# Kernel optimization log

Hardware: AMD Instinct MI355X
Metric: run time of the kernel (lower is better)

Reference implementation:

```python
import jax, jax.numpy as jnp
import numpy as np

# ---- layer_param constants (ihmehimmeli alpha-synapse defaults, see shape_source) ----
K_NO_SPIKE = 1000.0
DECAY_RATE = 1.0          # K in exp(K*t)
DECAY_RATE_INV = 1.0
FIRE_THRESHOLD = 1.0
IN_FEATURES = 1024
OUT_FEATURES = 512
N_PULSE = 10
BATCH = 32
MIN_W_ARG = -0.3678794411714423  # -1/e, domain boundary of Lambert W0


def lambertw0(x):
    """Principal branch Lambert W on [-1/e, 0], via Halley iterations."""
    e = jnp.exp(1.0)
    # series init near the branch point, w ~= x for small |x|
    w = jnp.where(x < -0.25,
                  -1.0 + jnp.sqrt(jnp.maximum(2.0 * (1.0 + e * x), 0.0)),
                  x * (1.0 - x))
    def halley(w, _):
        ew = jnp.exp(w)
        f = w * ew - x
        denom = ew * (w + 1.0) - (w + 2.0) * f / (2.0 * (w + 1.0) + 1e-12)
        w = w - f / (denom + 1e-12)
        return w, None
    w, _ = jax.lax.scan(halley, w, None, length=12)
    return w


def _alpha_solve(act, weight):
    """Causal-set cumulative spike-time solve for alpha synapses.
    act: [B,N] input spike times, weight: [O,N].
    V(t) = e^{-K t} (A t - B) with A = sum w e^{K t_i}, B = sum w t_i e^{K t_i};
    threshold crossing: t* = B/A - W0(-theta*K/A * e^{K B/A})/K,
    valid if t* lies between the last included and the next input spike.
    """
    order = jnp.argsort(act, axis=1)                             # [B,N]
    t_s = jnp.take_along_axis(act, order, axis=1)                # sorted spike times
    valid_in = t_s < K_NO_SPIKE
    z = jnp.where(valid_in, jnp.exp(DECAY_RATE * t_s), 0.0)      # exp of valid sorted spikes
    w_s = weight[:, order].transpose(1, 0, 2)                    # [B,O,N] weights in sorted order
    A_c = jnp.cumsum(w_s * z[:, None, :], axis=2)                # causal-set cumulative A
    B_c = jnp.cumsum(w_s * (z * t_s)[:, None, :], axis=2)        # causal-set cumulative B
    A_pos = A_c > 1e-10
    A_safe = jnp.where(A_pos, A_c, 1.0)
    b_over_a = B_c / A_safe
    arg = -FIRE_THRESHOLD * DECAY_RATE / A_safe * jnp.exp(jnp.minimum(DECAY_RATE * b_over_a, 80.0))
    lam_ok = A_pos & (arg >= MIN_W_ARG)
    wl = lambertw0(jnp.clip(arg, MIN_W_ARG, 0.0))
    t_cand = b_over_a - wl * DECAY_RATE_INV
    next_t = jnp.concatenate([t_s[:, 1:], jnp.full_like(t_s[:, :1], K_NO_SPIKE)], axis=1)
    valid = (lam_ok & valid_in[:, None, :]
             & (t_cand >= t_s[:, None, :]) & (t_cand <= next_t[:, None, :]))
    k_star = jnp.argmax(valid, axis=2)                           # first causal set that fires
    spiked = jnp.any(valid, axis=2)
    take = lambda m: jnp.take_along_axis(m, k_star[:, :, None], axis=2)[:, :, 0]
    spike_time = jnp.where(spiked, take(t_cand), K_NO_SPIKE)
    A = jnp.where(spiked, take(A_c), 1.0)
    Bv = jnp.where(spiked, take(B_c), 0.0)
    Wv = jnp.where(spiked, take(wl), 0.0)
    rank = jnp.argsort(order, axis=1)                            # position of each input in sorted order
    causal = rank[:, None, :] <= k_star[:, :, None]              # [B,O,N]
    return spike_time, A, Bv, Wv, causal


def setup_inputs() -> dict:
    key = jax.random.key(0)
    k1, k2 = jax.random.split(key)
    x = jax.random.uniform(k1, (BATCH, IN_FEATURES), dtype=jnp.float32)
    std = float(np.sqrt(2.0 / (IN_FEATURES + OUT_FEATURES)))
    weight = std * 7.0 + std * jax.random.normal(k2, (OUT_FEATURES, IN_FEATURES + N_PULSE), dtype=jnp.float32)
    pulse = jnp.linspace(0.0, 1.0, N_PULSE + 2, dtype=jnp.float32)[1:-1]
    return {"x": x, "weight": weight, "pulse": pulse}


def reference(x, weight, pulse):
    act = jnp.concatenate([x, jnp.broadcast_to(pulse[None, :], (x.shape[0], N_PULSE))], axis=1)
    spike_time, _, _, _, _ = _alpha_solve(act, weight)
    return spike_time
```

## Files before the change

kernel.cpp:

```cpp
#include <hip/hip_runtime.h>
#include <math.h>
#include <limits.h>

#define IN_FEATURES 1024
#define OUT_FEATURES 512
#define N_PULSE 10
#define NCOL 1034
#define BATCH 32
#define MIN_W_ARG -0.3678794411714423

#define NSEG 16
#define SEG 66
#define SCAN (NSEG * SEG)
#define TBLN 1088

#define OFF_TS  (TBLN * 4)
#define OFF_Z   (TBLN * 8)
#define OFF_ZT  (TBLN * 16)
#define TBL_BYTES (TBLN * 24)

#define PREP_T_BLOCKS 136
#define PREP_R_PARTS 5
#define PREP_BLOCKS (PREP_T_BLOCKS + BATCH * PREP_R_PARTS)

__global__ __launch_bounds__(256, 1) void prep_kernel(
        const float* __restrict__ w, float* __restrict__ wT,
        const float* __restrict__ x, const float* __restrict__ pulse,
        char* __restrict__ tbl) {
    __shared__ char smem_u[64 * 65 * 4];
    const int tid = threadIdx.x;

    if (blockIdx.x < PREP_T_BLOCKS) {
        float (*tile)[65] = (float (*)[65])smem_u;
        const int n0 = (blockIdx.x % 17) * 64;
        const int o0 = (blockIdx.x / 17) * 64;
        const int tx = tid & 63, ty = tid >> 6;
        #pragma unroll
        for (int r = 0; r < 16; ++r) {
            int ol = r * 4 + ty, n = n0 + tx;
            if (n < NCOL) tile[ol][tx] = w[(o0 + ol) * NCOL + n];
        }
        __syncthreads();
        #pragma unroll
        for (int r = 0; r < 16; ++r) {
            int nl = r * 4 + ty, n = n0 + nl;
            if (n < NCOL) wT[n * OUT_FEATURES + o0 + tx] = tile[tx][nl];
        }
    } else {
        unsigned long long* sk = (unsigned long long*)smem_u;
        float* keyf = (float*)(smem_u + TBLN * 8);
        const int rb = blockIdx.x - PREP_T_BLOCKS;
        const int b = rb / PREP_R_PARTS, part = rb % PREP_R_PARTS;

        for (int e = tid; e < TBLN; e += 256) {
            if (e < NCOL) {
                float t = (e < IN_FEATURES) ? x[b * IN_FEATURES + e]
                                            : pulse[e - IN_FEATURES];
                unsigned u = __float_as_uint(t);
                u = (u & 0x80000000u) ? ~u : (u | 0x80000000u);
                sk[e] = ((unsigned long long)u << 11) | (unsigned)e;
                keyf[e] = t;
            } else {
                sk[e] = 0xFFFFFFFFFFFFFFFFULL;
            }
        }
        __syncthreads();

        char* base = tbl + b * TBL_BYTES;
        int*    ordg = (int*)base;
        float*  tsg  = (float*)(base + OFF_TS);
        double* zg   = (double*)(base + OFF_Z);
        double* ztg  = (double*)(base + OFF_ZT);

        const int e = part * 256 + tid;
        if (e < NCOL) {
            unsigned long long mk = sk[e];
            int r = 0;
            for (int j0 = 0; j0 < TBLN; j0 += 16) {
                unsigned long long c[16];
                #pragma unroll
                for (int i = 0; i < 16; ++i) c[i] = sk[j0 + i];
                #pragma unroll
                for (int i = 0; i < 16; ++i) r += (c[i] < mk);
            }
            float t = keyf[e];
            double zv = exp((double)t);
            ordg[r] = e; tsg[r] = t; zg[r] = zv; ztg[r] = zv * (double)t;
        }
        if (part == PREP_R_PARTS - 1) {
            int p = 1024 + tid;
            if (p >= NCOL && p < TBLN) {
                ordg[p] = 0; tsg[p] = -1.0f; zg[p] = 0.0; ztg[p] = 0.0;
            }
        }
    }
}

__device__ __forceinline__ double lambertw0(double xx) {
    const double e = 2.718281828459045;
    double w = (xx < -0.25) ? (-1.0 + sqrt(fmax(2.0 * (1.0 + e * xx), 0.0)))
                            : xx * (1.0 - xx);
    #pragma unroll 4
    for (int i = 0; i < 12; ++i) {
        double ew = exp(w);
        double f  = w * ew - xx;
        double denom = ew * (w + 1.0) - (w + 2.0) * f / (2.0 * (w + 1.0) + 1e-12);
        w = w - f / (denom + 1e-12);
    }
    return w;
}

__global__ __launch_bounds__(1024) void solve_kernel(
        const float* __restrict__ wT,
        const char* __restrict__ tbl,
        float* __restrict__ out) {
    __shared__ char smem[TBL_BYTES];
    __shared__ double segA[NSEG * 64], segB[NSEG * 64];
    __shared__ int    sfk[NSEG * 64];
    __shared__ double sfA[NSEG * 64], sfB[NSEG * 64];

    const int b = blockIdx.x >> 3;
    const int o0 = (blockIdx.x & 7) << 6;
    const int wave = threadIdx.x >> 6;
    const int lane = threadIdx.x & 63;
    const int o = o0 + lane;

    {
        const uint4* g = (const uint4*)(tbl + b * TBL_BYTES);
        uint4* l = (uint4*)smem;
        for (int e = threadIdx.x; e < TBL_BYTES / 16; e += 1024) l[e] = g[e];
    }
    __syncthreads();
    const int*    ord_l = (const int*)smem;
    const float*  ts_l  = (const float*)(smem + OFF_TS);
    const double* z_l   = (const double*)(smem + OFF_Z);
    const double* zt_l  = (const double*)(smem + OFF_ZT);

    const int k0 = wave * SEG;

    {
        double a0 = 0.0, a1 = 0.0, b0 = 0.0, b1 = 0.0;
        for (int c = 0; c < SEG; c += 11) {
            int idx[11]; float buf[11];
            #pragma unroll
            for (int i = 0; i < 11; ++i) idx[i] = ord_l[k0 + c + i];
            #pragma unroll
            for (int i = 0; i < 11; ++i) buf[i] = wT[idx[i] * OUT_FEATURES + o];
            #pragma unroll
            for (int i = 0; i < 11; ++i) {
                double w = (double)buf[i];
                if (i & 1) { a1 = fma(w, z_l[k0 + c + i], a1);
                             b1 = fma(w, zt_l[k0 + c + i], b1); }
                else       { a0 = fma(w, z_l[k0 + c + i], a0);
                             b0 = fma(w, zt_l[k0 + c + i], b0); }
            }
        }
        segA[wave * 64 + lane] = a0 + a1;
        segB[wave * 64 + lane] = b0 + b1;
    }
    __syncthreads();

    {
        double A = 0.0, Bv = 0.0;
        for (int s = 0; s < wave; ++s) {
            A  += segA[s * 64 + lane];
            Bv += segB[s * 64 + lane];
        }
        int fk = INT_MAX; double fA = 0.0, fB = 0.0;
        for (int c = 0; c < SEG; c += 11) {
            int idx[11]; float buf[11];
            #pragma unroll
            for (int i = 0; i < 11; ++i) idx[i] = ord_l[k0 + c + i];
            #pragma unroll
            for (int i = 0; i < 11; ++i) buf[i] = wT[idx[i] * OUT_FEATURES + o];
            #pragma unroll
            for (int i = 0; i < 11; ++i) {
                int k = k0 + c + i;
                double w = (double)buf[i];
                A  = fma(w, z_l[k],  A);
                Bv = fma(w, zt_l[k], Bv);
                bool fire = (fk == INT_MAX) & (A > 1e-10) &
                            (fma(A, (double)ts_l[k + 1], -Bv) >= z_l[k + 1]);
                if (fire) { fk = k; fA = A; fB = Bv; }
            }
        }
        sfk[wave * 64 + lane] = fk;
        sfA[wave * 64 + lane] = fA;
        sfB[wave * 64 + lane] = fB;
    }
    __syncthreads();

    if (wave == 0) {
        int gk = INT_MAX; double gA = 0.0, gB = 0.0;
        #pragma unroll
        for (int s = 0; s < NSEG; ++s) {
            int k = sfk[s * 64 + lane];
            if (k < gk) { gk = k; gA = sfA[s * 64 + lane]; gB = sfB[s * 64 + lane]; }
        }
        bool done = (gk < NCOL);

        double AA, BB, tk, tn;
        bool have;
        if (done) {
            AA = gA; BB = gB;
            tk = (double)ts_l[gk];
            tn = (double)ts_l[gk + 1];
            have = true;
        } else {
            double tA = 0.0, tB = 0.0;
            #pragma unroll
            for (int s = 0; s < NSEG; ++s) { tA += segA[s * 64 + lane]; tB += segB[s * 64 + lane]; }
            AA = tA; BB = tB;
            tk = (double)ts_l[NCOL - 1];
            tn = 1000.0;
            have = (AA > 1e-10);
        }

        float result = 1000.0f;
        bool need_fb = false;
        if (have) {
            double boa = BB / AA;
            double arg = -exp(fmin(boa, 80.0)) / AA;
            if (arg >= MIN_W_ARG) {
                double wl = lambertw0(fmin(fmax(arg, MIN_W_ARG), 0.0));
                double tc = boa - wl;
                if (tc >= tk && tc <= tn) result = (float)tc;
                else need_fb = done;
            } else need_fb = done;
        }

        if (__ballot(need_fb) != 0ULL) {
            double A2 = gA, B2 = gB;
            for (int k = gk + 1; k < NCOL && k >= 0; ++k) {
                if (!need_fb) break;
                double w = (double)wT[ord_l[k] * OUT_FEATURES + o];
                A2 = fma(w, z_l[k], A2);
                B2 = fma(w, zt_l[k], B2);
                if (!(A2 > 1e-10)) continue;
                double tkk = (double)ts_l[k];
                double tnn = (k == NCOL - 1) ? 1000.0 : (double)ts_l[k + 1];
                double boa = B2 / A2;
                double arg = -exp(fmin(boa, 80.0)) / A2;
                if (arg >= MIN_W_ARG) {
                    double wl = lambertw0(fmin(fmax(arg, MIN_W_ARG), 0.0));
                    double tc = boa - wl;
                    if (tc >= tkk && tc <= tnn) { result = (float)tc; need_fb = false; }
                }
            }
        }
        out[b * OUT_FEATURES + o] = result;
    }
}

extern "C" void kernel_launch(void* const* d_in, const int* in_sizes, int n_in,
                              void* d_out, int out_size, void* d_ws, size_t ws_size,
                              hipStream_t stream) {
    const float* x      = (const float*)d_in[0];
    const float* weight = (const float*)d_in[1];
    const float* pulse  = (const float*)d_in[2];
    float* out = (float*)d_out;

    char* ws = (char*)d_ws;
    float* wT = (float*)ws;
    char*  tbl = ws + (size_t)NCOL * OUT_FEATURES * 4;

    hipLaunchKernelGGL(prep_kernel, dim3(PREP_BLOCKS), dim3(256), 0, stream,
                       weight, wT, x, pulse, tbl);
    hipLaunchKernelGGL(solve_kernel, dim3(BATCH * OUT_FEATURES / 64), dim3(1024), 0, stream,
                       wT, tbl, out);
}
```

Baseline: 91.48 us.

## Replace full rank-count sort with bucketed counting sort in prep kernel

Swaps the O(N^2) all-pairs rank count (spread over 5 blocks per batch row) for a bucket sort in one block per batch: histogram into 1024 buckets by value, prefix-scan, scatter, then rank each element only against others in its own bucket. This cuts the per-element comparison work in the prep stage. The bucket mapping assumes inputs lie in [0,1), which holds for uniform x and pulse values, and heavily skewed distributions would degrade it back toward quadratic within a bucket. Ties are still broken by index, so the ordering stays the same.

```diff
diff --git a/kernel.cpp b/kernel.cpp
--- a/kernel.cpp
+++ b/kernel.cpp
@@ -11,7 +11,6 @@
 
 #define NSEG 16
 #define SEG 66
-#define SCAN (NSEG * SEG)
 #define TBLN 1088
 
 #define OFF_TS  (TBLN * 4)
@@ -20,14 +19,21 @@
 #define TBL_BYTES (TBLN * 24)
 
 #define PREP_T_BLOCKS 136
-#define PREP_R_PARTS 5
-#define PREP_BLOCKS (PREP_T_BLOCKS + BATCH * PREP_R_PARTS)
+#define PREP_BLOCKS (PREP_T_BLOCKS + BATCH)
+
+#define R_KM   0
+#define R_KF   4136
+#define R_SIDX 8272
+#define R_BASE 12408
+#define R_RUN  16508
+#define R_PS   20604
+#define R_BYTES 21632
 
 __global__ __launch_bounds__(256, 1) void prep_kernel(
         const float* __restrict__ w, float* __restrict__ wT,
         const float* __restrict__ x, const float* __restrict__ pulse,
         char* __restrict__ tbl) {
-    __shared__ char smem_u[64 * 65 * 4];
+    __shared__ __align__(16) char smem_u[R_BYTES];
     const int tid = threadIdx.x;
 
     if (blockIdx.x < PREP_T_BLOCKS) {
@@ -47,51 +53,79 @@
             if (n < NCOL) wT[n * OUT_FEATURES + o0 + tx] = tile[tx][nl];
         }
     } else {
-        unsigned long long* sk = (unsigned long long*)smem_u;
-        float* keyf = (float*)(smem_u + TBLN * 8);
-        const int rb = blockIdx.x - PREP_T_BLOCKS;
-        const int b = rb / PREP_R_PARTS, part = rb % PREP_R_PARTS;
-
-        for (int e = tid; e < TBLN; e += 256) {
-            if (e < NCOL) {
-                float t = (e < IN_FEATURES) ? x[b * IN_FEATURES + e]
-                                            : pulse[e - IN_FEATURES];
-                unsigned u = __float_as_uint(t);
-                u = (u & 0x80000000u) ? ~u : (u | 0x80000000u);
-                sk[e] = ((unsigned long long)u << 11) | (unsigned)e;
-                keyf[e] = t;
-            } else {
-                sk[e] = 0xFFFFFFFFFFFFFFFFULL;
+        unsigned*  km   = (unsigned*)(smem_u + R_KM);
+        float*     kf   = (float*)(smem_u + R_KF);
+        int*       sidx = (int*)(smem_u + R_SIDX);
+        int*       base = (int*)(smem_u + R_BASE);
+        int*       run  = (int*)(smem_u + R_RUN);
+        int*       ps   = (int*)(smem_u + R_PS);
+        const int b = blockIdx.x - PREP_T_BLOCKS;
+
+        for (int e = tid; e < NCOL; e += 256) {
+            float t = (e < IN_FEATURES) ? x[b * IN_FEATURES + e]
+                                        : pulse[e - IN_FEATURES];
+            kf[e] = t;
+            unsigned u = __float_as_uint(t);
+            km[e] = (u & 0x80000000u) ? ~u : (u | 0x80000000u);
+        }
+        for (int i = tid; i < 1024; i += 256) run[i] = 0;
+        __syncthreads();
+
+        for (int e = tid; e < NCOL; e += 256) {
+            int bk = min(1023, max(0, (int)(kf[e] * 1024.0f)));
+            atomicAdd(&run[bk], 1);
+        }
+        __syncthreads();
+
+        int c4[4], v = 0;
+        #pragma unroll
+        for (int j = 0; j < 4; ++j) { c4[j] = run[4 * tid + j]; v += c4[j]; }
+        ps[tid] = v;
+        __syncthreads();
+        for (int off = 1; off < 256; off <<= 1) {
+            int xv = (tid >= off) ? ps[tid - off] : 0;
+            __syncthreads();
+            ps[tid] += xv;
+            __syncthreads();
+        }
+        int ex = ps[tid] - v;
+        #pragma unroll
+        for (int j = 0; j < 4; ++j) { base[4 * tid + j] = ex; ex += c4[j]; }
+        if (tid == 255) base[1024] = ex;
+        __syncthreads();
+        for (int i = tid; i < 1024; i += 256) run[i] = base[i];
+        __syncthreads();
+
+        for (int e = tid; e < NCOL; e += 256) {
+            int bk = min(1023, max(0, (int)(kf[e] * 1024.0f)));
+            int slot = atomicAdd(&run[bk], 1);
+            sidx[slot] = e;
+        }
+        __syncthreads();
+
+        char* gb = tbl + b * TBL_BYTES;
+        int*    ordg = (int*)gb;
+        float*  tsg  = (float*)(gb + OFF_TS);
+        double* zg   = (double*)(gb + OFF_Z);
+        double* ztg  = (double*)(gb + OFF_ZT);
+
+        for (int s = tid; s < NCOL; s += 256) {
+            int e = sidx[s];
+            float t = kf[e];
+            unsigned u = km[e];
+            int bk = min(1023, max(0, (int)(t * 1024.0f)));
+            int lo = base[bk], hi = base[bk + 1];
+            int r = lo;
+            for (int j = lo; j < hi; ++j) {
+                int ej = sidx[j];
+                unsigned uj = km[ej];
+                r += (uj < u) || (uj == u && ej < e);
             }
-        }
-        __syncthreads();
-
-        char* base = tbl + b * TBL_BYTES;
-        int*    ordg = (int*)base;
-        float*  tsg  = (float*)(base + OFF_TS);
-        double* zg   = (double*)(base + OFF_Z);
-        double* ztg  = (double*)(base + OFF_ZT);
-
-        const int e = part * 256 + tid;
-        if (e < NCOL) {
-            unsigned long long mk = sk[e];
-            int r = 0;
-            for (int j0 = 0; j0 < TBLN; j0 += 16) {
-                unsigned long long c[16];
-                #pragma unroll
-                for (int i = 0; i < 16; ++i) c[i] = sk[j0 + i];
-                #pragma unroll
-                for (int i = 0; i < 16; ++i) r += (c[i] < mk);
-            }
-            float t = keyf[e];
             double zv = exp((double)t);
             ordg[r] = e; tsg[r] = t; zg[r] = zv; ztg[r] = zv * (double)t;
         }
-        if (part == PREP_R_PARTS - 1) {
-            int p = 1024 + tid;
-            if (p >= NCOL && p < TBLN) {
-                ordg[p] = 0; tsg[p] = -1.0f; zg[p] = 0.0; ztg[p] = 0.0;
-            }
+        for (int p = NCOL + tid; p < TBLN; p += 256) {
+            ordg[p] = 0; tsg[p] = -1.0f; zg[p] = 0.0; ztg[p] = 0.0;
         }
     }
 }
```

New measurement: 85.67 us, median of 2. 1.07x faster.
